# Optimization experiments

Hardware: AMD Instinct MI355X
Metric: run time of the kernel (lower is better)

Reference implementation:

```python
import jax, jax.numpy as jnp
import numpy as np

B, Q, K, DQ, DK, DV, H = 16, 64, 512, 512, 512, 512, 256
MASK_VAL = -1e6


def setup_inputs() -> dict:
    key = jax.random.key(0)
    k1, k2, k3, k4, k5, k6, k7 = jax.random.split(key, 7)
    return {
        "queries": jax.random.normal(k1, (B, Q, DQ), dtype=jnp.float32),
        "keys": jax.random.normal(k2, (B, K, DK), dtype=jnp.float32),
        "values": jax.random.normal(k3, (B, K, DV), dtype=jnp.float32),
        "valid_lens": jax.random.randint(k4, (B,), 1, K + 1, dtype=jnp.int32),
        "Wq": jax.random.normal(k5, (DQ, H), dtype=jnp.float32) * (1.0 / np.sqrt(DQ)),
        "Wk": jax.random.normal(k6, (DK, H), dtype=jnp.float32) * (1.0 / np.sqrt(DK)),
        "Wv": jax.random.normal(k7, (H,), dtype=jnp.float32) * (1.0 / np.sqrt(H)),
    }


def reference(queries, keys, values, valid_lens, Wq, Wk, Wv):
    # Project queries and keys into the shared additive-attention space.
    q = jnp.einsum("bqd,dh->bqh", queries, Wq)   # [B,Q,H]
    k = jnp.einsum("bkd,dh->bkh", keys, Wk)      # [B,K,H]
    # Bahdanau additive scoring: tanh(q + k) projected to a scalar per (q,k).
    feats = jnp.tanh(q[:, :, None, :] + k[:, None, :, :])  # [B,Q,K,H]
    scores = jnp.einsum("bqkh,h->bqk", feats, Wv)           # [B,Q,K]
    # Masked softmax over the key axis (positions >= valid_len masked out).
    mask = jnp.arange(K)[None, None, :] < valid_lens[:, None, None]  # [B,1,K]
    scores = jnp.where(mask, scores, MASK_VAL)
    attn = jax.nn.softmax(scores, axis=-1)                  # [B,Q,K]
    # Dropout is identity in eval mode; weighted sum of values.
    return jnp.einsum("bqk,bkv->bqv", attn, values)         # [B,Q,DV]
```

## Files before the change

### kernel.cpp

```cpp
#include <hip/hip_runtime.h>

#define LOG2E 1.4426950408889634f
#define TWO_LOG2E 2.8853900817779268f

typedef __attribute__((ext_vector_type(8))) short short8;
typedef __attribute__((ext_vector_type(4))) float f32x4;

__device__ __forceinline__ float e2x(float v) {
    return __builtin_amdgcn_exp2f(v * TWO_LOG2E);
}

__device__ __forceinline__ void split2(float x, float y, unsigned& hi, unsigned& lo) {
    unsigned ux = __float_as_uint(x), uy = __float_as_uint(y);
    float hx = __uint_as_float(ux & 0xffff0000u);
    float hy = __uint_as_float(uy & 0xffff0000u);
    unsigned lx = __float_as_uint(x - hx), ly = __float_as_uint(y - hy);
    hi = (ux >> 16) | (uy & 0xffff0000u);
    lo = (lx >> 16) | (ly & 0xffff0000u);
}

__global__ __launch_bounds__(256) void wprep_kernel(const float* __restrict__ Wq,
                                                    const float* __restrict__ Wk,
                                                    ushort* __restrict__ Wq2T,
                                                    ushort* __restrict__ Wk2T) {
    __shared__ float T[64][65];
    const float* W  = blockIdx.z ? Wk : Wq;
    ushort* W2T     = blockIdx.z ? Wk2T : Wq2T;
    const int t  = threadIdx.x;
    const int k0 = blockIdx.x * 64;
    const int n0 = blockIdx.y * 64;
#pragma unroll
    for (int p = 0; p < 4; ++p) {
        int u  = t + p * 256;
        int kk = u >> 4;
        int nf = (u & 15) * 4;
        float4 w = *reinterpret_cast<const float4*>(&W[(size_t)(k0 + kk) * 256 + n0 + nf]);
        T[nf + 0][kk] = w.x; T[nf + 1][kk] = w.y;
        T[nf + 2][kk] = w.z; T[nf + 3][kk] = w.w;
    }
    __syncthreads();
#pragma unroll
    for (int p = 0; p < 4; ++p) {
        int u  = t + p * 256;
        int n  = u >> 4;
        int kf = (u & 15) * 4;
        float a = T[n][kf], b = T[n][kf + 1], c = T[n][kf + 2], d = T[n][kf + 3];
        unsigned h01, l01, h23, l23;
        split2(a, b, h01, l01);
        split2(c, d, h23, l23);
        int kg = k0 + kf;
        ushort* row = W2T + (size_t)(n0 + n) * 1536 + (kg >> 5) * 96 + (kg & 31);
        uint2 hi; hi.x = h01; hi.y = h23;
        uint2 lo; lo.x = l01; lo.y = l23;
        *reinterpret_cast<uint2*>(row)      = hi;
        *reinterpret_cast<uint2*>(row + 32) = hi;
        *reinterpret_cast<uint2*>(row + 64) = lo;
    }
}

__global__ __launch_bounds__(256) void mfma_proj_kernel(const float* __restrict__ queries,
                                                        const float* __restrict__ keys,
                                                        const ushort* __restrict__ Wq2T,
                                                        const ushort* __restrict__ Wk2T,
                                                        float* __restrict__ Eq,
                                                        float* __restrict__ Ekp) {
    __shared__ float smemf[4608];
    ushort* Ah = reinterpret_cast<ushort*>(smemf);
    ushort* Ws = reinterpret_cast<ushort*>(smemf) + 3072;

    const int t    = threadIdx.x;
    const int mt   = blockIdx.x;
    const int Nb   = blockIdx.y * 64;
    const bool isQ = mt < 32;
    const int mloc = (isQ ? mt : mt - 32) * 32;
    const float4* Asrc4 = reinterpret_cast<const float4*>(isQ ? queries : keys)
                        + (size_t)mloc * 128;
    const ushort* W2T = isQ ? Wq2T : Wk2T;

    const int ln15 = t & 15;
    const int q    = (t >> 4) & 3;
    const int w    = t >> 6;
    const int wn   = w * 16;
    const int am   = t >> 3;
    const int ak   = t & 7;

    const char* gB[3];
#pragma unroll
    for (int i = 0; i < 3; ++i) {
        int o   = i * 4096 + t * 16;
        int row = o / 192;
        int rem = o - row * 192;
        gB[i] = reinterpret_cast<const char*>(W2T) + (size_t)(Nb + row) * 3072 + rem;
    }

    f32x4 acc[2];
    acc[0] = (f32x4)0.0f;
    acc[1] = (f32x4)0.0f;

    float4 ra = Asrc4[(size_t)am * 128 + ak];

    for (int c = 0; c < 16; ++c) {
        __syncthreads();
#pragma unroll
        for (int i = 0; i < 3; ++i) {
            __builtin_amdgcn_global_load_lds(
                reinterpret_cast<const unsigned int*>(gB[i]),
                reinterpret_cast<unsigned int*>(
                    reinterpret_cast<char*>(Ah) + 6144 + i * 4096 + (t >> 6) * 1024),
                16, 0, 0);
            gB[i] += 192;
        }
        {
            unsigned h01, l01, h23, l23;
            split2(ra.x, ra.y, h01, l01);
            split2(ra.z, ra.w, h23, l23);
            uint2 hi; hi.x = h01; hi.y = h23;
            uint2 lo; lo.x = l01; lo.y = l23;
            ushort* row = Ah + am * 96 + ak * 4;
            *reinterpret_cast<uint2*>(row)      = hi;
            *reinterpret_cast<uint2*>(row + 32) = lo;
            *reinterpret_cast<uint2*>(row + 64) = hi;
        }
        if (c < 15) ra = Asrc4[(size_t)am * 128 + (c + 1) * 8 + ak];
        __syncthreads();
#pragma unroll
        for (int s = 0; s < 3; ++s) {
            short8 af[2], bf;
#pragma unroll
            for (int fm = 0; fm < 2; ++fm)
                af[fm] = *reinterpret_cast<const short8*>(
                    Ah + (fm * 16 + ln15) * 96 + s * 32 + q * 8);
            bf = *reinterpret_cast<const short8*>(
                Ws + (wn + ln15) * 96 + s * 32 + q * 8);
#pragma unroll
            for (int fm = 0; fm < 2; ++fm)
                acc[fm] = __builtin_amdgcn_mfma_f32_16x16x32_bf16(
                    af[fm], bf, acc[fm], 0, 0, 0);
        }
    }

    if (isQ) {
#pragma unroll
        for (int fm = 0; fm < 2; ++fm)
#pragma unroll
            for (int r = 0; r < 4; ++r) {
                int row = mloc + fm * 16 + q * 4 + r;
                int col = Nb + wn + ln15;
                Eq[(size_t)row * 256 + col] = e2x(acc[fm][r]);
            }
    } else {
        __syncthreads();
        float (*Cs)[33] = reinterpret_cast<float(*)[33]>(smemf);
#pragma unroll
        for (int fm = 0; fm < 2; ++fm)
#pragma unroll
            for (int r = 0; r < 4; ++r) {
                int m_l = fm * 16 + q * 4 + r;
                int n_l = wn + ln15;
                Cs[n_l][m_l] = acc[fm][r];
            }
        __syncthreads();
        const int b      = mloc >> 9;
        const int k0h    = (mloc & 511) >> 1;
        const int h2base = Nb >> 1;
        float4* out4 = reinterpret_cast<float4*>(Ekp);
#pragma unroll
        for (int p = 0; p < 2; ++p) {
            int u   = t + p * 256;
            int h2r = u >> 4;
            int kp  = u & 15;
            int kk  = kp * 2;
            float4 o;
            o.x = e2x(Cs[2 * h2r    ][kk    ]);
            o.y = e2x(Cs[2 * h2r + 1][kk    ]);
            o.z = e2x(Cs[2 * h2r    ][kk + 1]);
            o.w = e2x(Cs[2 * h2r + 1][kk + 1]);
            out4[(size_t)b * 32768 + (size_t)(h2base + h2r) * 256 + k0h + kp] = o;
        }
    }
}

__global__ __launch_bounds__(256) void score_raw_kernel(
        const float* __restrict__ Eq, const float* __restrict__ Ekp,
        const float* __restrict__ Wv, const int* __restrict__ valid_lens,
        float* __restrict__ scores) {
    __shared__ float Eqs[8][256];
    __shared__ float Wvs[256];
    __shared__ float Sh[4][8][64];
    const int t  = threadIdx.x;
    const int kb = blockIdx.x * 64;
    const int q0 = blockIdx.y * 8;
    const int b  = blockIdx.z;

    const float4* eq4 = reinterpret_cast<const float4*>(Eq + (size_t)(b * 64 + q0) * 256);
#pragma unroll
    for (int i = 0; i < 2; ++i) {
        int u = t + i * 256;
        *reinterpret_cast<float4*>(&Eqs[u >> 6][(u & 63) * 4]) = eq4[u];
    }
    Wvs[t] = Wv[t];
    __syncthreads();

    const int kl = t & 63;
    const int hh = t >> 6;
    const float2* ek2 = reinterpret_cast<const float2*>(Ekp)
                      + (size_t)b * 65536 + (size_t)(hh * 32) * 512 + kb + kl;

    float acc[8] = {0.f, 0.f, 0.f, 0.f, 0.f, 0.f, 0.f, 0.f};
#pragma unroll 4
    for (int i = 0; i < 32; ++i) {
        float2 ek = ek2[(size_t)i * 512];
        int h2 = hh * 32 + i;
        float2 wv = *reinterpret_cast<const float2*>(&Wvs[2 * h2]);
#pragma unroll
        for (int q = 0; q < 8; ++q) {
            float2 e = *reinterpret_cast<const float2*>(&Eqs[q][2 * h2]);
            float a0 = fmaf(e.x, ek.x, 1.0f);
            float a1 = fmaf(e.y, ek.y, 1.0f);
            float d  = a0 * a1;
            float n  = fmaf(wv.y, a0, wv.x * a1);
            acc[q] = fmaf(n, __builtin_amdgcn_rcpf(d), acc[q]);
        }
    }
#pragma unroll
    for (int q = 0; q < 8; ++q) Sh[hh][q][kl] = acc[q];
    __syncthreads();

    const int vl = valid_lens[b];
#pragma unroll
    for (int i = 0; i < 2; ++i) {
        int u = t + i * 256;
        int q = u >> 6, k = u & 63;
        float s = -2.0f * ((Sh[0][q][k] + Sh[1][q][k]) + (Sh[2][q][k] + Sh[3][q][k]));
        if (kb + k >= vl) s = -1e6f;
        scores[(size_t)(b * 64 + q0 + q) * 512 + kb + k] = s;
    }
}

__global__ __launch_bounds__(256) void pv_kernel(const float* __restrict__ scores,
                                                 const float* __restrict__ values,
                                                 float* __restrict__ out) {
    __shared__ __align__(16) float Ps[16][516];
    __shared__ __align__(16) float Vs[2][32][64];

    const int t  = threadIdx.x;
    const int b  = blockIdx.z;
    const int q0 = blockIdx.y * 16;
    const int vt = blockIdx.x;

    const float4* sc4 = reinterpret_cast<const float4*>(scores) + (size_t)(b * 64 + q0) * 128;
#pragma unroll
    for (int p = 0; p < 8; ++p) {
        int u  = t + p * 256;
        int qr = u >> 7;
        int c4 = u & 127;
        *reinterpret_cast<float4*>(&Ps[qr][c4 * 4]) = sc4[(size_t)qr * 128 + c4];
    }

    const char* vbase = reinterpret_cast<const char*>(values)
                      + ((size_t)b * 512 * 512 + (size_t)vt * 64) * 4
                      + (size_t)(t >> 4) * 2048 + (size_t)(t & 15) * 16;
    char* ldsV0 = reinterpret_cast<char*>(&Vs[0][0][0]) + (t >> 6) * 1024;

    const int lane = t & 63;
    const int w    = t >> 6;
    const int v4   = lane & 15;
    const int ksub = lane >> 4;

#pragma unroll
    for (int i = 0; i < 2; ++i)
        __builtin_amdgcn_global_load_lds(
            reinterpret_cast<const unsigned int*>(vbase + (size_t)i * 32768),
            reinterpret_cast<unsigned int*>(ldsV0 + i * 4096), 16, 0, 0);
    __syncthreads();

#pragma unroll
    for (int rr = 0; rr < 4; ++rr) {
        const int r = 4 * w + rr;
        float v[8];
        float m = -1e30f;
#pragma unroll
        for (int i = 0; i < 8; ++i) { v[i] = Ps[r][lane + i * 64]; m = fmaxf(m, v[i]); }
#pragma unroll
        for (int off = 32; off > 0; off >>= 1) m = fmaxf(m, __shfl_xor(m, off));
        float s = 0.f;
#pragma unroll
        for (int i = 0; i < 8; ++i) {
            v[i] = __builtin_amdgcn_exp2f((v[i] - m) * LOG2E);
            s += v[i];
        }
#pragma unroll
        for (int off = 32; off > 0; off >>= 1) s += __shfl_xor(s, off);
        float inv = 1.0f / s;
#pragma unroll
        for (int i = 0; i < 8; ++i) Ps[r][lane + i * 64] = v[i] * inv;
    }

    float4 acc[4];
#pragma unroll
    for (int r = 0; r < 4; ++r) acc[r] = make_float4(0.f, 0.f, 0.f, 0.f);

    for (int c = 0; c < 16; ++c) {
        if (c < 15) {
            char* dst = reinterpret_cast<char*>(&Vs[(c + 1) & 1][0][0]) + (t >> 6) * 1024;
            const char* src = vbase + (size_t)(c + 1) * 65536;
#pragma unroll
            for (int i = 0; i < 2; ++i)
                __builtin_amdgcn_global_load_lds(
                    reinterpret_cast<const unsigned int*>(src + (size_t)i * 32768),
                    reinterpret_cast<unsigned int*>(dst + i * 4096), 16, 0, 0);
        }

        const float (*V)[64] = Vs[c & 1];
#pragma unroll
        for (int kk = 0; kk < 2; ++kk) {
            int kb = kk * 16 + ksub * 4;
            float4 V0 = *reinterpret_cast<const float4*>(&V[kb + 0][v4 * 4]);
            float4 V1 = *reinterpret_cast<const float4*>(&V[kb + 1][v4 * 4]);
            float4 V2 = *reinterpret_cast<const float4*>(&V[kb + 2][v4 * 4]);
            float4 V3 = *reinterpret_cast<const float4*>(&V[kb + 3][v4 * 4]);
#pragma unroll
            for (int r = 0; r < 4; ++r) {
                float4 p = *reinterpret_cast<const float4*>(&Ps[4 * w + r][c * 32 + kb]);
                acc[r].x = fmaf(p.x, V0.x, acc[r].x); acc[r].y = fmaf(p.x, V0.y, acc[r].y);
                acc[r].z = fmaf(p.x, V0.z, acc[r].z); acc[r].w = fmaf(p.x, V0.w, acc[r].w);
                acc[r].x = fmaf(p.y, V1.x, acc[r].x); acc[r].y = fmaf(p.y, V1.y, acc[r].y);
                acc[r].z = fmaf(p.y, V1.z, acc[r].z); acc[r].w = fmaf(p.y, V1.w, acc[r].w);
                acc[r].x = fmaf(p.z, V2.x, acc[r].x); acc[r].y = fmaf(p.z, V2.y, acc[r].y);
                acc[r].z = fmaf(p.z, V2.z, acc[r].z); acc[r].w = fmaf(p.z, V2.w, acc[r].w);
                acc[r].x = fmaf(p.w, V3.x, acc[r].x); acc[r].y = fmaf(p.w, V3.y, acc[r].y);
                acc[r].z = fmaf(p.w, V3.z, acc[r].z); acc[r].w = fmaf(p.w, V3.w, acc[r].w);
            }
        }
        __syncthreads();
    }

#pragma unroll
    for (int off = 16; off <= 32; off <<= 1)
#pragma unroll
        for (int r = 0; r < 4; ++r) {
            acc[r].x += __shfl_xor(acc[r].x, off); acc[r].y += __shfl_xor(acc[r].y, off);
            acc[r].z += __shfl_xor(acc[r].z, off); acc[r].w += __shfl_xor(acc[r].w, off);
        }
    if (ksub == 0) {
        float4* out4 = reinterpret_cast<float4*>(out);
#pragma unroll
        for (int r = 0; r < 4; ++r)
            out4[(size_t)(b * 64 + q0 + 4 * w + r) * 128 + vt * 16 + v4] = acc[r];
    }
}

extern "C" void kernel_launch(void* const* d_in, const int* in_sizes, int n_in,
                              void* d_out, int out_size, void* d_ws, size_t ws_size,
                              hipStream_t stream) {
    (void)in_sizes; (void)n_in; (void)out_size; (void)ws_size;
    const float* queries    = (const float*)d_in[0];
    const float* keys       = (const float*)d_in[1];
    const float* values     = (const float*)d_in[2];
    const int*   valid_lens = (const int*)d_in[3];
    const float* Wq         = (const float*)d_in[4];
    const float* Wk         = (const float*)d_in[5];
    const float* Wv         = (const float*)d_in[6];
    float* out = (float*)d_out;

    float* ws     = (float*)d_ws;
    float* Eq     = ws;
    float* Ekp    = ws + 262144;
    float* scores = ws + 262144 + 2097152;
    ushort* Wq2T  = (ushort*)(ws + 2883584);
    ushort* Wk2T  = Wq2T + 393216;

    hipLaunchKernelGGL(wprep_kernel, dim3(8, 4, 2), dim3(256), 0, stream,
                       Wq, Wk, Wq2T, Wk2T);
    hipLaunchKernelGGL(mfma_proj_kernel, dim3(288, 4), dim3(256), 0, stream,
                       queries, keys, Wq2T, Wk2T, Eq, Ekp);
    hipLaunchKernelGGL(score_raw_kernel, dim3(8, 8, 16), dim3(256), 0, stream,
                       Eq, Ekp, Wv, valid_lens, scores);
    hipLaunchKernelGGL(pv_kernel, dim3(8, 4, 16), dim3(256), 0, stream,
                       scores, values, out);
}
```

Before: 139.3 us.

## Fuse score and PV into one kernel with atomic split-K accumulation

Merges the score kernel and the softmax/PV kernel into a single kernel, so the scores matrix is no longer written to and read back from workspace and one launch is dropped. Each block exponentiates its 64-key tile of scores without subtracting a row max and multiplies directly by values. It atomically adds the partial outputs and softmax denominators to global memory, and the last block per (batch, query-tile) normalizes via a counter. Zeroing of the output and of the counters is folded into the earlier kernels. The cost is heavy atomic traffic on the output, values read redundantly by every query tile, and reliance on scores staying small enough that exp without a max shift cannot overflow.

```diff
diff --git a/kernel.cpp b/kernel.cpp
--- a/kernel.cpp
+++ b/kernel.cpp
@@ -22,13 +22,22 @@
 __global__ __launch_bounds__(256) void wprep_kernel(const float* __restrict__ Wq,
                                                     const float* __restrict__ Wk,
                                                     ushort* __restrict__ Wq2T,
-                                                    ushort* __restrict__ Wk2T) {
+                                                    ushort* __restrict__ Wk2T,
+                                                    float* __restrict__ denom,
+                                                    int* __restrict__ counter) {
     __shared__ float T[64][65];
     const float* W  = blockIdx.z ? Wk : Wq;
     ushort* W2T     = blockIdx.z ? Wk2T : Wq2T;
     const int t  = threadIdx.x;
     const int k0 = blockIdx.x * 64;
     const int n0 = blockIdx.y * 64;
+
+    if (blockIdx.x == 0 && blockIdx.y == 0 && blockIdx.z == 0) {
+#pragma unroll
+        for (int i = 0; i < 4; ++i) denom[t + i * 256] = 0.0f;
+        if (t < 128) counter[t] = 0;
+    }
+
 #pragma unroll
     for (int p = 0; p < 4; ++p) {
         int u  = t + p * 256;
@@ -63,7 +72,8 @@
                                                         const ushort* __restrict__ Wq2T,
                                                         const ushort* __restrict__ Wk2T,
                                                         float* __restrict__ Eq,
-                                                        float* __restrict__ Ekp) {
+                                                        float* __restrict__ Ekp,
+                                                        float* __restrict__ outz) {
     __shared__ float smemf[4608];
     ushort* Ah = reinterpret_cast<ushort*>(smemf);
     ushort* Ws = reinterpret_cast<ushort*>(smemf) + 3072;
@@ -71,6 +81,13 @@
     const int t    = threadIdx.x;
     const int mt   = blockIdx.x;
     const int Nb   = blockIdx.y * 64;
+
+    {
+        int idx = (blockIdx.y * 288 + blockIdx.x) * 114 + t;
+        if (t < 114 && idx < 131072)
+            reinterpret_cast<float4*>(outz)[idx] = make_float4(0.f, 0.f, 0.f, 0.f);
+    }
+
     const bool isQ = mt < 32;
     const int mloc = (isQ ? mt : mt - 32) * 32;
     const float4* Asrc4 = reinterpret_cast<const float4*>(isQ ? queries : keys)
@@ -180,13 +197,16 @@
     }
 }
 
-__global__ __launch_bounds__(256) void score_raw_kernel(
+__global__ __launch_bounds__(256) void scorepv_kernel(
         const float* __restrict__ Eq, const float* __restrict__ Ekp,
         const float* __restrict__ Wv, const int* __restrict__ valid_lens,
-        float* __restrict__ scores) {
+        const float* __restrict__ values, float* __restrict__ out,
+        float* __restrict__ denom, int* __restrict__ counter) {
     __shared__ float Eqs[8][256];
     __shared__ float Wvs[256];
     __shared__ float Sh[4][8][64];
+    __shared__ float EsT[64][8];
+    __shared__ int   flag;
     const int t  = threadIdx.x;
     const int kb = blockIdx.x * 64;
     const int q0 = blockIdx.y * 8;
@@ -233,120 +253,68 @@
         int q = u >> 6, k = u & 63;
         float s = -2.0f * ((Sh[0][q][k] + Sh[1][q][k]) + (Sh[2][q][k] + Sh[3][q][k]));
         if (kb + k >= vl) s = -1e6f;
-        scores[(size_t)(b * 64 + q0 + q) * 512 + kb + k] = s;
-    }
-}
-
-__global__ __launch_bounds__(256) void pv_kernel(const float* __restrict__ scores,
-                                                 const float* __restrict__ values,
-                                                 float* __restrict__ out) {
-    __shared__ __align__(16) float Ps[16][516];
-    __shared__ __align__(16) float Vs[2][32][64];
-
-    const int t  = threadIdx.x;
-    const int b  = blockIdx.z;
-    const int q0 = blockIdx.y * 16;
-    const int vt = blockIdx.x;
-
-    const float4* sc4 = reinterpret_cast<const float4*>(scores) + (size_t)(b * 64 + q0) * 128;
-#pragma unroll
-    for (int p = 0; p < 8; ++p) {
-        int u  = t + p * 256;
-        int qr = u >> 7;
-        int c4 = u & 127;
-        *reinterpret_cast<float4*>(&Ps[qr][c4 * 4]) = sc4[(size_t)qr * 128 + c4];
-    }
-
-    const char* vbase = reinterpret_cast<const char*>(values)
-                      + ((size_t)b * 512 * 512 + (size_t)vt * 64) * 4
-                      + (size_t)(t >> 4) * 2048 + (size_t)(t & 15) * 16;
-    char* ldsV0 = reinterpret_cast<char*>(&Vs[0][0][0]) + (t >> 6) * 1024;
-
-    const int lane = t & 63;
-    const int w    = t >> 6;
-    const int v4   = lane & 15;
-    const int ksub = lane >> 4;
-
-#pragma unroll
-    for (int i = 0; i < 2; ++i)
-        __builtin_amdgcn_global_load_lds(
-            reinterpret_cast<const unsigned int*>(vbase + (size_t)i * 32768),
-            reinterpret_cast<unsigned int*>(ldsV0 + i * 4096), 16, 0, 0);
-    __syncthreads();
-
-#pragma unroll
-    for (int rr = 0; rr < 4; ++rr) {
-        const int r = 4 * w + rr;
-        float v[8];
-        float m = -1e30f;
-#pragma unroll
-        for (int i = 0; i < 8; ++i) { v[i] = Ps[r][lane + i * 64]; m = fmaxf(m, v[i]); }
-#pragma unroll
-        for (int off = 32; off > 0; off >>= 1) m = fmaxf(m, __shfl_xor(m, off));
-        float s = 0.f;
-#pragma unroll
-        for (int i = 0; i < 8; ++i) {
-            v[i] = __builtin_amdgcn_exp2f((v[i] - m) * LOG2E);
-            s += v[i];
-        }
-#pragma unroll
-        for (int off = 32; off > 0; off >>= 1) s += __shfl_xor(s, off);
-        float inv = 1.0f / s;
-#pragma unroll
-        for (int i = 0; i < 8; ++i) Ps[r][lane + i * 64] = v[i] * inv;
-    }
-
-    float4 acc[4];
-#pragma unroll
-    for (int r = 0; r < 4; ++r) acc[r] = make_float4(0.f, 0.f, 0.f, 0.f);
-
-    for (int c = 0; c < 16; ++c) {
-        if (c < 15) {
-            char* dst = reinterpret_cast<char*>(&Vs[(c + 1) & 1][0][0]) + (t >> 6) * 1024;
-            const char* src = vbase + (size_t)(c + 1) * 65536;
-#pragma unroll
-            for (int i = 0; i < 2; ++i)
-                __builtin_amdgcn_global_load_lds(
-                    reinterpret_cast<const unsigned int*>(src + (size_t)i * 32768),
-                    reinterpret_cast<unsigned int*>(dst + i * 4096), 16, 0, 0);
-        }
-
-        const float (*V)[64] = Vs[c & 1];
-#pragma unroll
-        for (int kk = 0; kk < 2; ++kk) {
-            int kb = kk * 16 + ksub * 4;
-            float4 V0 = *reinterpret_cast<const float4*>(&V[kb + 0][v4 * 4]);
-            float4 V1 = *reinterpret_cast<const float4*>(&V[kb + 1][v4 * 4]);
-            float4 V2 = *reinterpret_cast<const float4*>(&V[kb + 2][v4 * 4]);
-            float4 V3 = *reinterpret_cast<const float4*>(&V[kb + 3][v4 * 4]);
-#pragma unroll
-            for (int r = 0; r < 4; ++r) {
-                float4 p = *reinterpret_cast<const float4*>(&Ps[4 * w + r][c * 32 + kb]);
-                acc[r].x = fmaf(p.x, V0.x, acc[r].x); acc[r].y = fmaf(p.x, V0.y, acc[r].y);
-                acc[r].z = fmaf(p.x, V0.z, acc[r].z); acc[r].w = fmaf(p.x, V0.w, acc[r].w);
-                acc[r].x = fmaf(p.y, V1.x, acc[r].x); acc[r].y = fmaf(p.y, V1.y, acc[r].y);
-                acc[r].z = fmaf(p.y, V1.z, acc[r].z); acc[r].w = fmaf(p.y, V1.w, acc[r].w);
-                acc[r].x = fmaf(p.z, V2.x, acc[r].x); acc[r].y = fmaf(p.z, V2.y, acc[r].y);
-                acc[r].z = fmaf(p.z, V2.z, acc[r].z); acc[r].w = fmaf(p.z, V2.w, acc[r].w);
-                acc[r].x = fmaf(p.w, V3.x, acc[r].x); acc[r].y = fmaf(p.w, V3.y, acc[r].y);
-                acc[r].z = fmaf(p.w, V3.z, acc[r].z); acc[r].w = fmaf(p.w, V3.w, acc[r].w);
-            }
-        }
-        __syncthreads();
-    }
-
-#pragma unroll
-    for (int off = 16; off <= 32; off <<= 1)
-#pragma unroll
-        for (int r = 0; r < 4; ++r) {
-            acc[r].x += __shfl_xor(acc[r].x, off); acc[r].y += __shfl_xor(acc[r].y, off);
-            acc[r].z += __shfl_xor(acc[r].z, off); acc[r].w += __shfl_xor(acc[r].w, off);
-        }
-    if (ksub == 0) {
-        float4* out4 = reinterpret_cast<float4*>(out);
-#pragma unroll
-        for (int r = 0; r < 4; ++r)
-            out4[(size_t)(b * 64 + q0 + 4 * w + r) * 128 + vt * 16 + v4] = acc[r];
+        float E = __builtin_amdgcn_exp2f(s * LOG2E);
+        EsT[k][q] = E;
+        float r = E;
+#pragma unroll
+        for (int off = 32; off > 0; off >>= 1) r += __shfl_xor(r, off);
+        if (kl == 0) unsafeAtomicAdd(&denom[b * 64 + q0 + q], r);
+    }
+    __syncthreads();
+
+    const int half = t >> 7;
+    const int f4c  = t & 127;
+    const float4* Vb = reinterpret_cast<const float4*>(values)
+                     + (size_t)(b * 512 + kb) * 128 + f4c;
+    float4 o[4];
+#pragma unroll
+    for (int j = 0; j < 4; ++j) o[j] = make_float4(0.f, 0.f, 0.f, 0.f);
+
+#pragma unroll 4
+    for (int k = 0; k < 64; ++k) {
+        float4 V = Vb[(size_t)k * 128];
+        float4 e = *reinterpret_cast<const float4*>(&EsT[k][4 * half]);
+        o[0].x = fmaf(e.x, V.x, o[0].x); o[0].y = fmaf(e.x, V.y, o[0].y);
+        o[0].z = fmaf(e.x, V.z, o[0].z); o[0].w = fmaf(e.x, V.w, o[0].w);
+        o[1].x = fmaf(e.y, V.x, o[1].x); o[1].y = fmaf(e.y, V.y, o[1].y);
+        o[1].z = fmaf(e.y, V.z, o[1].z); o[1].w = fmaf(e.y, V.w, o[1].w);
+        o[2].x = fmaf(e.z, V.x, o[2].x); o[2].y = fmaf(e.z, V.y, o[2].y);
+        o[2].z = fmaf(e.z, V.z, o[2].z); o[2].w = fmaf(e.z, V.w, o[2].w);
+        o[3].x = fmaf(e.w, V.x, o[3].x); o[3].y = fmaf(e.w, V.y, o[3].y);
+        o[3].z = fmaf(e.w, V.z, o[3].z); o[3].w = fmaf(e.w, V.w, o[3].w);
+    }
+
+    {
+        float* ob = out + (size_t)(b * 64 + q0 + 4 * half) * 512 + f4c * 4;
+#pragma unroll
+        for (int j = 0; j < 4; ++j) {
+            unsafeAtomicAdd(&ob[(size_t)j * 512 + 0], o[j].x);
+            unsafeAtomicAdd(&ob[(size_t)j * 512 + 1], o[j].y);
+            unsafeAtomicAdd(&ob[(size_t)j * 512 + 2], o[j].z);
+            unsafeAtomicAdd(&ob[(size_t)j * 512 + 3], o[j].w);
+        }
+    }
+
+    __threadfence();
+    __syncthreads();
+    if (t == 0) flag = (atomicAdd(&counter[b * 8 + blockIdx.y], 1) == 7) ? 1 : 0;
+    __syncthreads();
+    if (flag) {
+#pragma unroll
+        for (int p = 0; p < 4; ++p) {
+            int u = t + p * 256;
+            int q = u >> 7;
+            int c = u & 127;
+            float dv   = unsafeAtomicAdd(&denom[b * 64 + q0 + q], 0.0f);
+            float invd = __builtin_amdgcn_rcpf(dv);
+            float* pb = out + (size_t)(b * 64 + q0 + q) * 512 + c * 4;
+            float x0 = unsafeAtomicAdd(&pb[0], 0.0f);
+            float x1 = unsafeAtomicAdd(&pb[1], 0.0f);
+            float x2 = unsafeAtomicAdd(&pb[2], 0.0f);
+            float x3 = unsafeAtomicAdd(&pb[3], 0.0f);
+            pb[0] = x0 * invd; pb[1] = x1 * invd;
+            pb[2] = x2 * invd; pb[3] = x3 * invd;
+        }
     }
 }
 
@@ -366,16 +334,15 @@
     float* ws     = (float*)d_ws;
     float* Eq     = ws;
     float* Ekp    = ws + 262144;
-    float* scores = ws + 262144 + 2097152;
+    float* denom  = ws + 2359296;
+    int*   counter= (int*)(ws + 2360320);
     ushort* Wq2T  = (ushort*)(ws + 2883584);
     ushort* Wk2T  = Wq2T + 393216;
 
     hipLaunchKernelGGL(wprep_kernel, dim3(8, 4, 2), dim3(256), 0, stream,
-                       Wq, Wk, Wq2T, Wk2T);
+                       Wq, Wk, Wq2T, Wk2T, denom, counter);
     hipLaunchKernelGGL(mfma_proj_kernel, dim3(288, 4), dim3(256), 0, stream,
-                       queries, keys, Wq2T, Wk2T, Eq, Ekp);
-    hipLaunchKernelGGL(score_raw_kernel, dim3(8, 8, 16), dim3(256), 0, stream,
-                       Eq, Ekp, Wv, valid_lens, scores);
-    hipLaunchKernelGGL(pv_kernel, dim3(8, 4, 16), dim3(256), 0, stream,
-                       scores, values, out);
-}
+                       queries, keys, Wq2T, Wk2T, Eq, Ekp, out);
+    hipLaunchKernelGGL(scorepv_kernel, dim3(8, 8, 16), dim3(256), 0, stream,
+                       Eq, Ekp, Wv, valid_lens, values, out, denom, counter);
+}
```

Result: slower. 465.6 us (+234.2%).
